# Performance work log

Hardware: AMD Instinct MI355X
Metric: run time of the kernel (lower is better)

## Reference

```python
import jax, jax.numpy as jnp
import numpy as np

N_NODES = 100000
N_EDGES = 1600000
D_IN = 64


def _graph_conv(x, edge_src, edge_dst, W, b, n_nodes):
    # gather source features along edges, mean-aggregate at destinations,
    # then linear transform + ReLU (standard GraphConv semantics)
    msgs = x[edge_src]  # [E, d]
    agg = jax.ops.segment_sum(msgs, edge_dst, num_segments=n_nodes)  # [N, d]
    deg = jax.ops.segment_sum(jnp.ones((edge_src.shape[0],), x.dtype), edge_dst,
                              num_segments=n_nodes)  # [N]
    agg = agg / jnp.maximum(deg, 1.0)[:, None]
    return jax.nn.relu(agg @ W + b)


def setup_inputs() -> dict:
    key = jax.random.key(0)
    ks = jax.random.split(key, 6)
    node_features = jax.random.normal(ks[0], (N_NODES, D_IN), dtype=jnp.float32)
    edge_src = jax.random.randint(ks[1], (N_EDGES,), 0, N_NODES)
    edge_dst = jax.random.randint(ks[2], (N_EDGES,), 0, N_NODES)
    W1 = jax.random.normal(ks[3], (D_IN, 64), dtype=jnp.float32) * (1.0 / np.sqrt(D_IN))
    b1 = jnp.zeros((64,), jnp.float32)
    W2 = jax.random.normal(ks[4], (64, 32), dtype=jnp.float32) * (1.0 / np.sqrt(64))
    b2 = jnp.zeros((32,), jnp.float32)
    Wd = jax.random.normal(ks[5], (1, 1), dtype=jnp.float32)
    bd = jnp.zeros((1,), jnp.float32)
    return {"node_features": node_features, "edge_src": edge_src, "edge_dst": edge_dst,
            "W1": W1, "b1": b1, "W2": W2, "b2": b2, "Wd": Wd, "bd": bd}


def reference(node_features, edge_src, edge_dst, W1, b1, W2, b2, Wd, bd):
    n_nodes = node_features.shape[0]
    x = _graph_conv(node_features, edge_src, edge_dst, W1, b1, n_nodes)  # [N, 64]
    x = _graph_conv(x, edge_src, edge_dst, W2, b2, n_nodes)              # [N, 32]
    x = jnp.mean(x, axis=1, keepdims=True)                               # [N, 1]
    return jax.nn.sigmoid(x @ Wd + bd)                                   # [N, 1]
```

## Files before the change

kernel.cpp:

```cpp
#include <hip/hip_runtime.h>
#include <hip/hip_bf16.h>

#define N_NODES 100000
#define N_EDGES 1600000
#define N_PAD   100096
#define BSHIFT  7
#define NBUCKET 782
#define BCAP    3072
#define EPB     2048
#define ZROW1   N_NODES
#define ZROW2   (2 * N_NODES)

__device__ __forceinline__ unsigned short f32_to_bf16(float f) {
    unsigned int u = __float_as_uint(f);
    unsigned int r = (u + 0x7fffu + ((u >> 16) & 1u)) >> 16;
    return (unsigned short)r;
}
__device__ __forceinline__ float bf16_lo(unsigned int p) {
    return __uint_as_float(p << 16);
}
__device__ __forceinline__ float bf16_hi(unsigned int p) {
    return __uint_as_float(p & 0xffff0000u);
}

__global__ void __launch_bounds__(256) bucket_scatter_lds(
    const int* __restrict__ src, const int* __restrict__ dst,
    int* __restrict__ bcur, unsigned int* __restrict__ tmp, int n_edges) {
    __shared__ int lh[1024];
    int t = threadIdx.x;
    int e0 = blockIdx.x * EPB;
    int e1 = min(e0 + EPB, n_edges);
    for (int i = t; i < 1024; i += 256) lh[i] = 0;
    __syncthreads();
    int ls[8], ld[8];
    #pragma unroll
    for (int j = 0; j < 8; j++) {
        int e = e0 + t + j * 256;
        if (e < e1) {
            ls[j] = src[e];
            ld[j] = dst[e];
            atomicAdd(&lh[ld[j] >> BSHIFT], 1);
        }
    }
    __syncthreads();
    for (int i = t; i < NBUCKET; i += 256) {
        int c = lh[i];
        lh[i] = (c > 0) ? atomicAdd(&bcur[i], c) : 0;
    }
    __syncthreads();
    #pragma unroll
    for (int j = 0; j < 8; j++) {
        int e = e0 + t + j * 256;
        if (e < e1) {
            int s = ls[j], d = ld[j];
            int b = d >> BSHIFT;
            int p = atomicAdd(&lh[b], 1);
            if (p < BCAP)
                tmp[(size_t)b * BCAP + p] = ((unsigned)s << BSHIFT) | (unsigned)(d & 127);
        }
    }
}

__global__ void __launch_bounds__(256) bucket_to_csr(
    const unsigned int* __restrict__ tmp, const int* __restrict__ bcur,
    int2* __restrict__ meta, int* __restrict__ col, int n_nodes) {
    __shared__ int nh[128];
    __shared__ int npref[128];
    int b = blockIdx.x;
    int t = threadIdx.x;
    int m = min(bcur[b], BCAP);
    int cbase = b * BCAP;
    if (t < 128) nh[t] = 0;
    __syncthreads();
    const unsigned int* te = tmp + (size_t)b * BCAP;
    for (int i = t; i < m; i += 256) atomicAdd(&nh[te[i] & 127], 1);
    __syncthreads();
    if (t < 128) npref[t] = nh[t];
    __syncthreads();
    for (int off = 1; off < 128; off <<= 1) {
        int u = (t < 128 && t >= off) ? npref[t - off] : 0;
        __syncthreads();
        if (t < 128) npref[t] += u;
        __syncthreads();
    }
    if (t < 128) {
        int node = (b << BSHIFT) + t;
        int ex = npref[t] - nh[t];
        if (node < n_nodes) meta[node] = make_int2(cbase + ex, nh[t]);
        nh[t] = cbase + ex;
    }
    __syncthreads();
    for (int i = t; i < m; i += 256) {
        unsigned int e = te[i];
        int pos = atomicAdd(&nh[e & 127], 1);
        col[pos] = (int)(e >> BSHIFT);
    }
}

__global__ void __launch_bounds__(256) gemm_n64(const float4* __restrict__ X4,
                                                const float* __restrict__ W,
                                                unsigned short* __restrict__ Y, int M) {
    __shared__ float sx[64][65];
    __shared__ float sw[64 * 64];
    int t = threadIdx.x;
    int base = blockIdx.x * 64;
    for (int i = t; i < 64 * 16; i += 256) {
        int r = i >> 4, c4 = i & 15;
        int row = base + r;
        float4 v = make_float4(0.f, 0.f, 0.f, 0.f);
        if (row < M) v = X4[(size_t)row * 16 + c4];
        sx[r][c4 * 4 + 0] = v.x; sx[r][c4 * 4 + 1] = v.y;
        sx[r][c4 * 4 + 2] = v.z; sx[r][c4 * 4 + 3] = v.w;
    }
    float4* sw4 = (float4*)sw;
    const float4* W4 = (const float4*)W;
    for (int i = t; i < 64 * 16; i += 256) sw4[i] = W4[i];
    __syncthreads();

    int tm = t & 15;
    int tn = t >> 4;
    float acc[4][4] = {{0.f}};
    #pragma unroll 8
    for (int k = 0; k < 64; k++) {
        float4 b = sw4[k * 16 + tn];
        float a0 = sx[tm * 4 + 0][k], a1 = sx[tm * 4 + 1][k];
        float a2 = sx[tm * 4 + 2][k], a3 = sx[tm * 4 + 3][k];
        acc[0][0] = fmaf(a0, b.x, acc[0][0]); acc[0][1] = fmaf(a0, b.y, acc[0][1]);
        acc[0][2] = fmaf(a0, b.z, acc[0][2]); acc[0][3] = fmaf(a0, b.w, acc[0][3]);
        acc[1][0] = fmaf(a1, b.x, acc[1][0]); acc[1][1] = fmaf(a1, b.y, acc[1][1]);
        acc[1][2] = fmaf(a1, b.z, acc[1][2]); acc[1][3] = fmaf(a1, b.w, acc[1][3]);
        acc[2][0] = fmaf(a2, b.x, acc[2][0]); acc[2][1] = fmaf(a2, b.y, acc[2][1]);
        acc[2][2] = fmaf(a2, b.z, acc[2][2]); acc[2][3] = fmaf(a2, b.w, acc[2][3]);
        acc[3][0] = fmaf(a3, b.x, acc[3][0]); acc[3][1] = fmaf(a3, b.y, acc[3][1]);
        acc[3][2] = fmaf(a3, b.z, acc[3][2]); acc[3][3] = fmaf(a3, b.w, acc[3][3]);
    }
    #pragma unroll
    for (int i = 0; i < 4; i++) {
        int row = base + tm * 4 + i;
        if (row < M) {
            ushort4 p;
            p.x = f32_to_bf16(acc[i][0]); p.y = f32_to_bf16(acc[i][1]);
            p.z = f32_to_bf16(acc[i][2]); p.w = f32_to_bf16(acc[i][3]);
            *(ushort4*)&Y[(size_t)row * 64 + tn * 4] = p;
        }
    }
}

__global__ void __launch_bounds__(256) gemm_n32(const float4* __restrict__ X4,
                                                const float* __restrict__ W,
                                                unsigned short* __restrict__ Z, int M) {
    __shared__ float sx[128][65];
    __shared__ float sw[64 * 32];
    int t = threadIdx.x;
    int base = blockIdx.x * 128;
    for (int i = t; i < 128 * 16; i += 256) {
        int r = i >> 4, c4 = i & 15;
        int row = base + r;
        float4 v = make_float4(0.f, 0.f, 0.f, 0.f);
        if (row < M) v = X4[(size_t)row * 16 + c4];
        sx[r][c4 * 4 + 0] = v.x; sx[r][c4 * 4 + 1] = v.y;
        sx[r][c4 * 4 + 2] = v.z; sx[r][c4 * 4 + 3] = v.w;
    }
    float4* sw4 = (float4*)sw;
    const float4* W4 = (const float4*)W;
    for (int i = t; i < 64 * 8; i += 256) sw4[i] = W4[i];
    __syncthreads();

    int tm = t & 31;
    int tn = t >> 5;
    float acc[4][4] = {{0.f}};
    #pragma unroll 8
    for (int k = 0; k < 64; k++) {
        float4 b = sw4[k * 8 + tn];
        float a0 = sx[tm * 4 + 0][k], a1 = sx[tm * 4 + 1][k];
        float a2 = sx[tm * 4 + 2][k], a3 = sx[tm * 4 + 3][k];
        acc[0][0] = fmaf(a0, b.x, acc[0][0]); acc[0][1] = fmaf(a0, b.y, acc[0][1]);
        acc[0][2] = fmaf(a0, b.z, acc[0][2]); acc[0][3] = fmaf(a0, b.w, acc[0][3]);
        acc[1][0] = fmaf(a1, b.x, acc[1][0]); acc[1][1] = fmaf(a1, b.y, acc[1][1]);
        acc[1][2] = fmaf(a1, b.z, acc[1][2]); acc[1][3] = fmaf(a1, b.w, acc[1][3]);
        acc[2][0] = fmaf(a2, b.x, acc[2][0]); acc[2][1] = fmaf(a2, b.y, acc[2][1]);
        acc[2][2] = fmaf(a2, b.z, acc[2][2]); acc[2][3] = fmaf(a2, b.w, acc[2][3]);
        acc[3][0] = fmaf(a3, b.x, acc[3][0]); acc[3][1] = fmaf(a3, b.y, acc[3][1]);
        acc[3][2] = fmaf(a3, b.z, acc[3][2]); acc[3][3] = fmaf(a3, b.w, acc[3][3]);
    }
    #pragma unroll
    for (int i = 0; i < 4; i++) {
        int row = base + tm * 4 + i;
        if (row < M) {
            ushort4 p;
            p.x = f32_to_bf16(acc[i][0]); p.y = f32_to_bf16(acc[i][1]);
            p.z = f32_to_bf16(acc[i][2]); p.w = f32_to_bf16(acc[i][3]);
            *(ushort4*)&Z[(size_t)row * 32 + tn * 4] = p;
        }
    }
}

__global__ void __launch_bounds__(256) gather_relu64(
    const uint4* __restrict__ Y4, const int2* __restrict__ meta,
    const int* __restrict__ col, const float* __restrict__ b1,
    float4* __restrict__ H4, int n_nodes) {
    int n = blockIdx.x * 4 + (threadIdx.x >> 6);
    if (n >= n_nodes) return;
    int lane = threadIdx.x & 63;
    int g = lane >> 3;
    int c = lane & 7;
    int2 md = meta[n];
    int beg = md.x;
    int d = md.y;
    int dm1 = max(d - 1, 0);

    float acc[8] = {0.f, 0.f, 0.f, 0.f, 0.f, 0.f, 0.f, 0.f};
    for (int i = 0; i < d; i += 32) {
        int i0 = i + g;
        int i1 = i0 + 8;
        int i2 = i0 + 16;
        int i3 = i0 + 24;
        int t0 = col[beg + min(i0, dm1)];
        int t1 = col[beg + min(i1, dm1)];
        int t2 = col[beg + min(i2, dm1)];
        int t3 = col[beg + min(i3, dm1)];
        int s0 = (i0 < d) ? t0 : ZROW1;
        int s1 = (i1 < d) ? t1 : ZROW1;
        int s2 = (i2 < d) ? t2 : ZROW1;
        int s3 = (i3 < d) ? t3 : ZROW1;
        uint4 v0 = Y4[(size_t)s0 * 8 + c];
        uint4 v1 = Y4[(size_t)s1 * 8 + c];
        uint4 v2 = Y4[(size_t)s2 * 8 + c];
        uint4 v3 = Y4[(size_t)s3 * 8 + c];
        acc[0] += (bf16_lo(v0.x) + bf16_lo(v1.x)) + (bf16_lo(v2.x) + bf16_lo(v3.x));
        acc[1] += (bf16_hi(v0.x) + bf16_hi(v1.x)) + (bf16_hi(v2.x) + bf16_hi(v3.x));
        acc[2] += (bf16_lo(v0.y) + bf16_lo(v1.y)) + (bf16_lo(v2.y) + bf16_lo(v3.y));
        acc[3] += (bf16_hi(v0.y) + bf16_hi(v1.y)) + (bf16_hi(v2.y) + bf16_hi(v3.y));
        acc[4] += (bf16_lo(v0.z) + bf16_lo(v1.z)) + (bf16_lo(v2.z) + bf16_lo(v3.z));
        acc[5] += (bf16_hi(v0.z) + bf16_hi(v1.z)) + (bf16_hi(v2.z) + bf16_hi(v3.z));
        acc[6] += (bf16_lo(v0.w) + bf16_lo(v1.w)) + (bf16_lo(v2.w) + bf16_lo(v3.w));
        acc[7] += (bf16_hi(v0.w) + bf16_hi(v1.w)) + (bf16_hi(v2.w) + bf16_hi(v3.w));
    }
    #pragma unroll
    for (int m = 8; m <= 32; m <<= 1) {
        #pragma unroll
        for (int q = 0; q < 8; q++) acc[q] += __shfl_xor(acc[q], m);
    }
    float inv = 1.0f / fmaxf((float)d, 1.0f);
    const float4* b1_4 = (const float4*)b1;
    float4 ba = b1_4[c * 2], bb = b1_4[c * 2 + 1];
    if (g == 0) {
        float4 o0, o1;
        o0.x = fmaxf(fmaf(acc[0], inv, ba.x), 0.f);
        o0.y = fmaxf(fmaf(acc[1], inv, ba.y), 0.f);
        o0.z = fmaxf(fmaf(acc[2], inv, ba.z), 0.f);
        o0.w = fmaxf(fmaf(acc[3], inv, ba.w), 0.f);
        o1.x = fmaxf(fmaf(acc[4], inv, bb.x), 0.f);
        o1.y = fmaxf(fmaf(acc[5], inv, bb.y), 0.f);
        o1.z = fmaxf(fmaf(acc[6], inv, bb.z), 0.f);
        o1.w = fmaxf(fmaf(acc[7], inv, bb.w), 0.f);
        H4[(size_t)n * 16 + c * 2]     = o0;
        H4[(size_t)n * 16 + c * 2 + 1] = o1;
    }
}

__global__ void __launch_bounds__(256) gather_final32(
    const uint4* __restrict__ Z4, const int2* __restrict__ meta,
    const int* __restrict__ col, const float* __restrict__ b2,
    const float* __restrict__ Wd, const float* __restrict__ bd,
    float* __restrict__ out, int n_nodes) {
    int n = blockIdx.x * 4 + (threadIdx.x >> 6);
    if (n >= n_nodes) return;
    int lane = threadIdx.x & 63;
    int g = lane >> 2;
    int c = lane & 3;
    int2 md = meta[n];
    int beg = md.x;
    int d = md.y;
    int dm1 = max(d - 1, 0);

    float acc[8] = {0.f, 0.f, 0.f, 0.f, 0.f, 0.f, 0.f, 0.f};
    for (int i = 0; i < d; i += 32) {
        int i0 = i + g;
        int i1 = i0 + 16;
        int t0 = col[beg + min(i0, dm1)];
        int t1 = col[beg + min(i1, dm1)];
        int s0 = (i0 < d) ? t0 : ZROW2;
        int s1 = (i1 < d) ? t1 : ZROW2;
        uint4 v0 = Z4[(size_t)s0 * 4 + c];
        uint4 v1 = Z4[(size_t)s1 * 4 + c];
        acc[0] += bf16_lo(v0.x) + bf16_lo(v1.x);
        acc[1] += bf16_hi(v0.x) + bf16_hi(v1.x);
        acc[2] += bf16_lo(v0.y) + bf16_lo(v1.y);
        acc[3] += bf16_hi(v0.y) + bf16_hi(v1.y);
        acc[4] += bf16_lo(v0.z) + bf16_lo(v1.z);
        acc[5] += bf16_hi(v0.z) + bf16_hi(v1.z);
        acc[6] += bf16_lo(v0.w) + bf16_lo(v1.w);
        acc[7] += bf16_hi(v0.w) + bf16_hi(v1.w);
    }
    #pragma unroll
    for (int m = 4; m <= 32; m <<= 1) {
        #pragma unroll
        for (int q = 0; q < 8; q++) acc[q] += __shfl_xor(acc[q], m);
    }
    float inv = 1.0f / fmaxf((float)d, 1.0f);
    const float4* b2_4 = (const float4*)b2;
    float4 ba = b2_4[c * 2], bb = b2_4[c * 2 + 1];
    float local = 0.f;
    local += fmaxf(fmaf(acc[0], inv, ba.x), 0.f);
    local += fmaxf(fmaf(acc[1], inv, ba.y), 0.f);
    local += fmaxf(fmaf(acc[2], inv, ba.z), 0.f);
    local += fmaxf(fmaf(acc[3], inv, ba.w), 0.f);
    local += fmaxf(fmaf(acc[4], inv, bb.x), 0.f);
    local += fmaxf(fmaf(acc[5], inv, bb.y), 0.f);
    local += fmaxf(fmaf(acc[6], inv, bb.z), 0.f);
    local += fmaxf(fmaf(acc[7], inv, bb.w), 0.f);
    local += __shfl_xor(local, 1);
    local += __shfl_xor(local, 2);
    if (lane == 0) {
        float z = fmaf(local * (1.0f / 32.0f), Wd[0], bd[0]);
        out[n] = 1.0f / (1.0f + __expf(-z));
    }
}

extern "C" void kernel_launch(void* const* d_in, const int* in_sizes, int n_in,
                              void* d_out, int out_size, void* d_ws, size_t ws_size,
                              hipStream_t stream) {
    const float* x    = (const float*)d_in[0];
    const int*   esrc = (const int*)d_in[1];
    const int*   edst = (const int*)d_in[2];
    const float* W1   = (const float*)d_in[3];
    const float* b1   = (const float*)d_in[4];
    const float* W2   = (const float*)d_in[5];
    const float* b2   = (const float*)d_in[6];
    const float* Wd   = (const float*)d_in[7];
    const float* bd   = (const float*)d_in[8];
    float* out = (float*)d_out;

    int* bcur    = (int*)d_ws;
    int2* meta   = (int2*)(bcur + 1024);
    int* col     = (int*)(meta + N_PAD);
    float* h     = (float*)(col + (size_t)NBUCKET * BCAP + 64);
    unsigned int* tmp = (unsigned int*)h;
    unsigned short* y  = (unsigned short*)(h + (size_t)N_NODES * 64);
    unsigned short* z2 = y;

    hipMemsetAsync((void*)bcur, 0, 1024 * sizeof(int), stream);
    hipMemsetAsync((void*)(y + (size_t)N_NODES * 64), 0, 128, stream);

    bucket_scatter_lds<<<(N_EDGES + EPB - 1) / EPB, 256, 0, stream>>>(
        esrc, edst, bcur, tmp, N_EDGES);
    bucket_to_csr<<<NBUCKET, 256, 0, stream>>>(tmp, bcur, meta, col, N_NODES);

    gemm_n64<<<(N_NODES + 63) / 64, 256, 0, stream>>>((const float4*)x, W1, y, N_NODES);
    gather_relu64<<<(N_NODES + 3) / 4, 256, 0, stream>>>(
        (const uint4*)y, meta, col, b1, (float4*)h, N_NODES);
    gemm_n32<<<(N_NODES + 127) / 128, 256, 0, stream>>>((const float4*)h, W2, z2, N_NODES);
    gather_final32<<<(N_NODES + 3) / 4, 256, 0, stream>>>(
        (const uint4*)z2, meta, col, b2, Wd, bd, out, N_NODES);
}
```

Before: 248.6 us.

## Replace bucketed LDS CSR build with global atomic count-scan-place CSR

The CSR construction changes from a two-kernel bucket scatter with fixed-capacity buckets to a classic count/scan/place pipeline. Degrees are counted with global atomics, then two scan levels build per-node offsets, and edges are placed with per-node global atomics. This removes the bucket capacity cap, so overflow can no longer drop edges, and it makes col compact. In exchange it adds three small launches and does scattered global atomics per edge, in place of LDS-local atomics followed by a coalesced bucket-local scatter.

```diff
diff --git a/kernel.cpp b/kernel.cpp
--- a/kernel.cpp
+++ b/kernel.cpp
@@ -4,10 +4,7 @@
 #define N_NODES 100000
 #define N_EDGES 1600000
 #define N_PAD   100096
-#define BSHIFT  7
 #define NBUCKET 782
-#define BCAP    3072
-#define EPB     2048
 #define ZROW1   N_NODES
 #define ZROW2   (2 * N_NODES)
 
@@ -23,77 +20,79 @@
     return __uint_as_float(p & 0xffff0000u);
 }
 
-__global__ void __launch_bounds__(256) bucket_scatter_lds(
+__global__ void __launch_bounds__(256) degree_count(
+    const int* __restrict__ dst, int* __restrict__ cnt, int n_edges) {
+    int e0 = blockIdx.x * 1024;
+    int t = threadIdx.x;
+    #pragma unroll
+    for (int j = 0; j < 4; j++) {
+        int e = e0 + t + j * 256;
+        if (e < n_edges) atomicAdd(&cnt[dst[e]], 1);
+    }
+}
+
+__global__ void __launch_bounds__(128) bucket_sum(
+    const int* __restrict__ cnt, int* __restrict__ bsum) {
+    __shared__ int s[128];
+    int b = blockIdx.x, t = threadIdx.x;
+    s[t] = cnt[b * 128 + t];
+    __syncthreads();
+    if (t < 64) {
+        int x = s[t] + s[t + 64];
+        #pragma unroll
+        for (int m = 32; m; m >>= 1) x += __shfl_down(x, m);
+        if (t == 0) bsum[b] = x;
+    }
+}
+
+__global__ void __launch_bounds__(1024) scan_buckets(
+    const int* __restrict__ bsum, int* __restrict__ boff) {
+    __shared__ int s[1024];
+    int t = threadIdx.x;
+    int v = (t < NBUCKET) ? bsum[t] : 0;
+    s[t] = v;
+    __syncthreads();
+    for (int off = 1; off < 1024; off <<= 1) {
+        int u = (t >= off) ? s[t - off] : 0;
+        __syncthreads();
+        s[t] += u;
+        __syncthreads();
+    }
+    if (t < NBUCKET) boff[t] = s[t] - v;
+}
+
+__global__ void __launch_bounds__(128) node_offsets(
+    const int* __restrict__ cnt, const int* __restrict__ boff,
+    int2* __restrict__ meta, int* __restrict__ cur, int n_nodes) {
+    __shared__ int s[128];
+    int b = blockIdx.x, t = threadIdx.x;
+    int n = b * 128 + t;
+    int c = cnt[n];
+    s[t] = c;
+    __syncthreads();
+    for (int off = 1; off < 128; off <<= 1) {
+        int u = (t >= off) ? s[t - off] : 0;
+        __syncthreads();
+        s[t] += u;
+        __syncthreads();
+    }
+    int begin = boff[b] + s[t] - c;
+    if (n < n_nodes) { meta[n] = make_int2(begin, c); cur[n] = begin; }
+}
+
+__global__ void __launch_bounds__(256) place_edges(
     const int* __restrict__ src, const int* __restrict__ dst,
-    int* __restrict__ bcur, unsigned int* __restrict__ tmp, int n_edges) {
-    __shared__ int lh[1024];
-    int t = threadIdx.x;
-    int e0 = blockIdx.x * EPB;
-    int e1 = min(e0 + EPB, n_edges);
-    for (int i = t; i < 1024; i += 256) lh[i] = 0;
-    __syncthreads();
-    int ls[8], ld[8];
-    #pragma unroll
-    for (int j = 0; j < 8; j++) {
+    int* __restrict__ cur, int* __restrict__ col, int n_edges) {
+    int e0 = blockIdx.x * 1024;
+    int t = threadIdx.x;
+    #pragma unroll
+    for (int j = 0; j < 4; j++) {
         int e = e0 + t + j * 256;
-        if (e < e1) {
-            ls[j] = src[e];
-            ld[j] = dst[e];
-            atomicAdd(&lh[ld[j] >> BSHIFT], 1);
+        if (e < n_edges) {
+            int d = dst[e];
+            int pos = atomicAdd(&cur[d], 1);
+            col[pos] = src[e];
         }
-    }
-    __syncthreads();
-    for (int i = t; i < NBUCKET; i += 256) {
-        int c = lh[i];
-        lh[i] = (c > 0) ? atomicAdd(&bcur[i], c) : 0;
-    }
-    __syncthreads();
-    #pragma unroll
-    for (int j = 0; j < 8; j++) {
-        int e = e0 + t + j * 256;
-        if (e < e1) {
-            int s = ls[j], d = ld[j];
-            int b = d >> BSHIFT;
-            int p = atomicAdd(&lh[b], 1);
-            if (p < BCAP)
-                tmp[(size_t)b * BCAP + p] = ((unsigned)s << BSHIFT) | (unsigned)(d & 127);
-        }
-    }
-}
-
-__global__ void __launch_bounds__(256) bucket_to_csr(
-    const unsigned int* __restrict__ tmp, const int* __restrict__ bcur,
-    int2* __restrict__ meta, int* __restrict__ col, int n_nodes) {
-    __shared__ int nh[128];
-    __shared__ int npref[128];
-    int b = blockIdx.x;
-    int t = threadIdx.x;
-    int m = min(bcur[b], BCAP);
-    int cbase = b * BCAP;
-    if (t < 128) nh[t] = 0;
-    __syncthreads();
-    const unsigned int* te = tmp + (size_t)b * BCAP;
-    for (int i = t; i < m; i += 256) atomicAdd(&nh[te[i] & 127], 1);
-    __syncthreads();
-    if (t < 128) npref[t] = nh[t];
-    __syncthreads();
-    for (int off = 1; off < 128; off <<= 1) {
-        int u = (t < 128 && t >= off) ? npref[t - off] : 0;
-        __syncthreads();
-        if (t < 128) npref[t] += u;
-        __syncthreads();
-    }
-    if (t < 128) {
-        int node = (b << BSHIFT) + t;
-        int ex = npref[t] - nh[t];
-        if (node < n_nodes) meta[node] = make_int2(cbase + ex, nh[t]);
-        nh[t] = cbase + ex;
-    }
-    __syncthreads();
-    for (int i = t; i < m; i += 256) {
-        unsigned int e = te[i];
-        int pos = atomicAdd(&nh[e & 127], 1);
-        col[pos] = (int)(e >> BSHIFT);
     }
 }
 
@@ -332,20 +331,24 @@
     const float* bd   = (const float*)d_in[8];
     float* out = (float*)d_out;
 
-    int* bcur    = (int*)d_ws;
-    int2* meta   = (int2*)(bcur + 1024);
-    int* col     = (int*)(meta + N_PAD);
-    float* h     = (float*)(col + (size_t)NBUCKET * BCAP + 64);
-    unsigned int* tmp = (unsigned int*)h;
+    int*  cnt  = (int*)d_ws;
+    int*  cur  = cnt + N_PAD;
+    int*  bsum = cur + N_PAD;
+    int*  boff = bsum + 1024;
+    int2* meta = (int2*)(boff + 1024);
+    int*  col  = (int*)(meta + N_PAD);
+    float* h   = (float*)(col + N_EDGES + 64);
     unsigned short* y  = (unsigned short*)(h + (size_t)N_NODES * 64);
     unsigned short* z2 = y;
 
-    hipMemsetAsync((void*)bcur, 0, 1024 * sizeof(int), stream);
+    hipMemsetAsync((void*)cnt, 0, N_PAD * sizeof(int), stream);
     hipMemsetAsync((void*)(y + (size_t)N_NODES * 64), 0, 128, stream);
 
-    bucket_scatter_lds<<<(N_EDGES + EPB - 1) / EPB, 256, 0, stream>>>(
-        esrc, edst, bcur, tmp, N_EDGES);
-    bucket_to_csr<<<NBUCKET, 256, 0, stream>>>(tmp, bcur, meta, col, N_NODES);
+    degree_count<<<(N_EDGES + 1023) / 1024, 256, 0, stream>>>(edst, cnt, N_EDGES);
+    bucket_sum  <<<NBUCKET, 128, 0, stream>>>(cnt, bsum);
+    scan_buckets<<<1, 1024, 0, stream>>>(bsum, boff);
+    node_offsets<<<NBUCKET, 128, 0, stream>>>(cnt, boff, meta, cur, N_NODES);
+    place_edges <<<(N_EDGES + 1023) / 1024, 256, 0, stream>>>(esrc, edst, cur, col, N_EDGES);
 
     gemm_n64<<<(N_NODES + 63) / 64, 256, 0, stream>>>((const float4*)x, W1, y, N_NODES);
     gather_relu64<<<(N_NODES + 3) / 4, 256, 0, stream>>>(
```

Measured after the change: 413.1 us. +66.1%, slower.
